# Performance work log

Hardware: AMD Instinct MI355X
Metric: run time of the kernel (lower is better)

Reference implementation:

```python
import jax, jax.numpy as jnp
import numpy as np

B, S = 4, 4096          # batch, tokens (64x64 SAM ViT-H grid)
DIN, DOUT = 1280, 3840  # qkv linear dims
RANK = 16
NUM_SHARED = 1
NUM_ROUTED = 6
TOP_K = 3


def setup_inputs() -> dict:
    key = jax.random.key(0)
    ks = jax.random.split(key, 9)
    s = 0.02
    return {
        "x": jax.random.normal(ks[0], (B, S, DIN), dtype=jnp.float32),
        "base_w": jax.random.normal(ks[1], (DIN, DOUT), dtype=jnp.float32) * s,
        "base_b": jax.random.normal(ks[2], (DOUT,), dtype=jnp.float32) * s,
        "shared_w1": jax.random.normal(ks[3], (NUM_SHARED, DIN, RANK), dtype=jnp.float32) * s,
        "shared_w2": jax.random.normal(ks[4], (NUM_SHARED, RANK, DOUT), dtype=jnp.float32) * s,
        "routed_w1": jax.random.normal(ks[5], (NUM_ROUTED, DIN, RANK), dtype=jnp.float32) * s,
        "routed_w2": jax.random.normal(ks[6], (NUM_ROUTED, RANK, DOUT), dtype=jnp.float32) * s,
        "router_w": jax.random.normal(ks[7], (DIN, NUM_ROUTED), dtype=jnp.float32) * s,
        "router_b": jax.random.normal(ks[8], (NUM_ROUTED,), dtype=jnp.float32) * s,
    }


def reference(x, base_w, base_b, shared_w1, shared_w2, routed_w1, routed_w2, router_w, router_b):
    b, s, din = x.shape
    # base linear runs under torch.no_grad() -> stop_gradient
    base = jax.lax.stop_gradient(jnp.einsum('bsi,io->bso', x, base_w) + base_b)
    # shared low-rank experts, summed over the shared set
    shared = jnp.einsum('bsi,eir,ero->bso', x, shared_w1, shared_w2)
    # router: softmax gates, top-k selection
    gates = jax.nn.softmax(x @ router_w + router_b, axis=-1)      # [B,S,E]
    topk_w, topk_idx = jax.lax.top_k(gates, TOP_K)                # [B,S,K]
    T = b * s
    xf = x.reshape(T, din)
    # combine weights: per-token weight for each expert (top-k indices are
    # distinct, so scatter-add reproduces the per-slot assignment exactly)
    cw = jnp.zeros((T, NUM_ROUTED), dtype=x.dtype).at[
        jnp.arange(T)[:, None], topk_idx.reshape(T, TOP_K)
    ].add(topk_w.reshape(T, TOP_K))                               # [T,E]
    # routed experts: contract rank and expert dims without materializing [T,E,DOUT]
    h = jnp.einsum('ti,eir->ter', xf, routed_w1)                  # [T,E,RANK]
    routed = jnp.einsum('ter,ero,te->to', h, routed_w2, cw).reshape(b, s, DOUT)
    return base + shared + routed
```

## Files before the change

### kernel.cpp

```cpp
#include <hip/hip_runtime.h>
#include <cstdint>
#include <cstddef>

#define DIN 1280
#define DOUT 3840
#define NEXP 6
#define RANK 16
#define TOKENS 16384
#define KPAD 1408
#define NLOW 128

typedef __bf16 bf16x8 __attribute__((ext_vector_type(8)));
typedef float f32x4 __attribute__((ext_vector_type(4)));
typedef unsigned short u16x8 __attribute__((ext_vector_type(8)));

#define SB() __builtin_amdgcn_sched_barrier(0)
#define BAR() __builtin_amdgcn_s_barrier()

__device__ __forceinline__ unsigned short f2bf(float f) {
    unsigned u = __builtin_bit_cast(unsigned, f);
    u += 0x7fff + ((u >> 16) & 1);
    return (unsigned short)(u >> 16);
}

__device__ __forceinline__ void async_load16(void* lds, const void* g) {
    __builtin_amdgcn_global_load_lds(
        (const __attribute__((address_space(1))) unsigned int*)g,
        (__attribute__((address_space(3))) unsigned int*)lds, 16, 0, 0);
}

__global__ void prep_w2t(const float* __restrict__ base_w,
                         const float* __restrict__ shared_w2,
                         const float* __restrict__ routed_w2,
                         unsigned short* __restrict__ WT) {
    __shared__ unsigned short tile[32][33];
    int k0 = blockIdx.x * 32, n0 = blockIdx.y * 32;
    int tx = threadIdx.x, ty = threadIdx.y;
#pragma unroll
    for (int j = 0; j < 4; j++) {
        int k = k0 + ty + j * 8;
        int n = n0 + tx;
        float v;
        if (k < DIN)            v = base_w[(size_t)k * DOUT + n];
        else if (k < DIN + 16)  v = shared_w2[(size_t)(k - DIN) * DOUT + n];
        else if (k < DIN + 112) v = routed_w2[(size_t)(k - DIN - 16) * DOUT + n];
        else                    v = 0.f;
        tile[ty + j * 8][tx] = f2bf(v);
    }
    __syncthreads();
#pragma unroll
    for (int j = 0; j < 4; j++) {
        int n = n0 + ty + j * 8;
        int k = k0 + tx;
        WT[(size_t)n * KPAD + k] = tile[tx][ty + j * 8];
    }
}

__global__ void prep_w1t(const float* __restrict__ shared_w1,
                         const float* __restrict__ routed_w1,
                         unsigned short* __restrict__ W1T) {
    __shared__ unsigned short tile[32][33];
    int k0 = blockIdx.x * 32, n0 = blockIdx.y * 32;
    int tx = threadIdx.x, ty = threadIdx.y;
#pragma unroll
    for (int j = 0; j < 4; j++) {
        int k = k0 + ty + j * 8;
        int n = n0 + tx;
        float v = 0.f;
        if (n < 16) v = shared_w1[k * RANK + n];
        else if (n < 112) {
            int jj = n - 16, e = jj >> 4, r = jj & 15;
            v = routed_w1[(size_t)e * DIN * RANK + k * RANK + r];
        }
        tile[ty + j * 8][tx] = f2bf(v);
    }
    __syncthreads();
#pragma unroll
    for (int j = 0; j < 4; j++) {
        int n = n0 + ty + j * 8;
        int k = k0 + tx;
        W1T[(size_t)n * DIN + k] = tile[tx][ty + j * 8];
    }
}

__global__ __launch_bounds__(256) void router_kernel(
    const float* __restrict__ x,
    const float* __restrict__ router_w,
    const float* __restrict__ router_b,
    unsigned short* __restrict__ A,
    float* __restrict__ cw) {
    int tid = threadIdx.x;
    size_t t0 = (size_t)blockIdx.x * 8;
    const float* xblk = x + t0 * DIN;
    unsigned short* Ablk = A + t0 * KPAD;

    for (int i = tid; i < 8 * (DIN / 8); i += 256) {
        int t = i / (DIN / 8), c = (i - t * (DIN / 8)) * 8;
        const float* xs = xblk + (size_t)t * DIN + c;
        f32x4 v0 = *(const f32x4*)xs;
        f32x4 v1 = *(const f32x4*)(xs + 4);
        u16x8 o;
#pragma unroll
        for (int j = 0; j < 4; j++) { o[j] = f2bf(v0[j]); o[4 + j] = f2bf(v1[j]); }
        *(u16x8*)&Ablk[(size_t)t * KPAD + c] = o;
    }
    if (tid < 128) {
        int t = tid >> 4, c = tid & 15;
        Ablk[t * KPAD + DIN + 112 + c] = 0;
    }

    int tg = tid >> 5, lj = tid & 31;
    const float* xt = xblk + (size_t)tg * DIN;
    float acc[6] = {0.f, 0.f, 0.f, 0.f, 0.f, 0.f};
    for (int k = lj; k < DIN; k += 32) {
        float xv = xt[k];
        const float* wr = router_w + k * NEXP;
#pragma unroll
        for (int e = 0; e < NEXP; e++) acc[e] = fmaf(xv, wr[e], acc[e]);
    }
#pragma unroll
    for (int off = 16; off > 0; off >>= 1)
#pragma unroll
        for (int e = 0; e < NEXP; e++) acc[e] += __shfl_xor(acc[e], off);

    float mx = -1e30f;
#pragma unroll
    for (int e = 0; e < NEXP; e++) { acc[e] += router_b[e]; mx = fmaxf(mx, acc[e]); }
    float g[6]; float s = 0.f;
#pragma unroll
    for (int e = 0; e < NEXP; e++) { g[e] = __expf(acc[e] - mx); s += g[e]; }
    float inv = 1.f / s;
    if (lj < NEXP) {
        float ge = g[lj];
        int cnt = 0;
#pragma unroll
        for (int e = 0; e < NEXP; e++) {
            if (e == lj) continue;
            if (g[e] > ge || (g[e] == ge && e < lj)) cnt++;
        }
        cw[(t0 + tg) * NEXP + lj] = (cnt < 3) ? ge * inv : 0.f;
    }
}

__global__ __launch_bounds__(256) void combine_kernel(
    const float* __restrict__ H, const float* __restrict__ cw,
    unsigned short* __restrict__ A) {
    int i = blockIdx.x * 256 + threadIdx.x;
    int t = i / 112, j = i - t * 112;
    float h = H[(size_t)t * NLOW + j] + H[(size_t)TOKENS * NLOW + (size_t)t * NLOW + j];
    float f = (j < 16) ? 1.0f : cw[t * NEXP + ((j - 16) >> 4)];
    A[(size_t)t * KPAD + DIN + j] = f2bf(f * h);
}

__global__ __launch_bounds__(256, 2) void gemm_small(
    const unsigned short* __restrict__ A,
    const unsigned short* __restrict__ BT,
    float* __restrict__ H) {
    __shared__ unsigned short ldsA[128 * 32];
    __shared__ unsigned short ldsB[128 * 32];
    const int KS = DIN / 2;
    int tid = threadIdx.x;
    int lane = tid & 63, wave = tid >> 6;
    int m0 = blockIdx.y * 128;
    int z = blockIdx.z;
    int wm = (wave >> 1) * 64, wn = (wave & 1) * 64;
    int lr = lane & 15, quad = lane >> 4;

    f32x4 acc[4][4] = {};
    const unsigned short* Abase = A + (size_t)m0 * KPAD + z * KS;
    const unsigned short* Bbase = BT + z * KS;
    float* Cbase = H + (size_t)z * TOKENS * NLOW;

    for (int k0 = 0; k0 < KS; k0 += 32) {
#pragma unroll
        for (int i = 0; i < 2; i++) {
            int c = i * 256 + tid;
            int row = c >> 2;
            int col = (c & 3) << 3;
            async_load16(&ldsA[(i * 256 + wave * 64) * 8],
                         Abase + (size_t)row * KPAD + k0 + col);
            async_load16(&ldsB[(i * 256 + wave * 64) * 8],
                         Bbase + (size_t)row * DIN + k0 + col);
        }
        __syncthreads();
        bf16x8 af[4], bf[4];
#pragma unroll
        for (int mi = 0; mi < 4; mi++)
            af[mi] = *(const bf16x8*)&ldsA[(wm + mi * 16 + lr) * 32 + quad * 8];
#pragma unroll
        for (int ni = 0; ni < 4; ni++)
            bf[ni] = *(const bf16x8*)&ldsB[(wn + ni * 16 + lr) * 32 + quad * 8];
#pragma unroll
        for (int mi = 0; mi < 4; mi++)
#pragma unroll
            for (int ni = 0; ni < 4; ni++)
                acc[mi][ni] = __builtin_amdgcn_mfma_f32_16x16x32_bf16(
                    af[mi], bf[ni], acc[mi][ni], 0, 0, 0);
        __syncthreads();
    }
#pragma unroll
    for (int ni = 0; ni < 4; ni++) {
        int gn = wn + ni * 16 + lr;
#pragma unroll
        for (int mi = 0; mi < 4; mi++) {
            int gm = m0 + wm + mi * 16 + quad * 4;
            f32x4 v = acc[mi][ni];
#pragma unroll
            for (int r = 0; r < 4; r++)
                Cbase[(size_t)(gm + r) * NLOW + gn] = v[r];
        }
    }
}


#define READ_AQ(AQ, MB) do { \
    AQ[0][0] = rdA(a_cur, (MB) + 0, 0); AQ[0][1] = rdA(a_cur, (MB) + 0, 1); \
    AQ[1][0] = rdA(a_cur, (MB) + 1, 0); AQ[1][1] = rdA(a_cur, (MB) + 1, 1); \
} while (0)

#define MFMA_QUAD(AQ, MB) do { \
    _Pragma("unroll") for (int ks_ = 0; ks_ < 2; ks_++) \
    _Pragma("unroll") for (int mq_ = 0; mq_ < 2; mq_++) \
    _Pragma("unroll") for (int ni_ = 0; ni_ < 4; ni_++) \
        acc[(MB) + mq_][ni_] = __builtin_amdgcn_mfma_f32_16x16x32_bf16( \
            AQ[mq_][ks_], bfr[ni_][ks_], acc[(MB) + mq_][ni_], 0, 0, 0); \
} while (0)

__global__ __launch_bounds__(512, 2) void gemm256(
    const unsigned short* __restrict__ A,
    const unsigned short* __restrict__ BT,
    const float* __restrict__ bias,
    float* __restrict__ C) {
    __shared__ unsigned short lA[2][256 * 64];
    __shared__ unsigned short lB[2][256 * 64];

    int tid = threadIdx.x;
    int lane = tid & 63, wave = tid >> 6;
    int bid = blockIdx.x;
    int xcd = bid & 7, lid = bid >> 3;
    int mt = xcd * 8 + (lid & 7);
    int nt = lid >> 3;
    int m0 = mt * 256, n0 = nt * 256;

    int wm = (wave >> 2) * 128, wn = (wave & 3) * 64;
    int lr = lane & 15, quad = lane >> 4;
    int swz = (lr & 7) << 4;

    int sr = lane >> 3;
    int sc = (lane & 7) ^ sr;
    const unsigned short* aSrc = A + (size_t)(m0 + wave * 32 + sr) * KPAD + sc * 8;
    const unsigned short* bSrc = BT + (size_t)(n0 + wave * 32 + sr) * KPAD + sc * 8;

    auto stA4 = [&](unsigned short* dst, int k0) {
#pragma unroll
        for (int i = 0; i < 4; i++)
            async_load16(dst + (size_t)(wave * 32 + i * 8) * 64,
                         aSrc + (size_t)(i * 8) * KPAD + k0);
    };
    auto stB1 = [&](unsigned short* dst, int k0, int i) {
        async_load16(dst + (size_t)(wave * 32 + i * 8) * 64,
                     bSrc + (size_t)(i * 8) * KPAD + k0);
    };
    auto rdA = [&](const unsigned short* base, int mi, int ks) -> bf16x8 {
        int row = wm + mi * 16 + lr;
        int off = row * 128 + (((ks << 6) | (quad << 4)) ^ swz);
        return *(const bf16x8*)((const char*)base + off);
    };
    auto rdB = [&](const unsigned short* base, int ni, int ks) -> bf16x8 {
        int row = wn + ni * 16 + lr;
        int off = row * 128 + (((ks << 6) | (quad << 4)) ^ swz);
        return *(const bf16x8*)((const char*)base + off);
    };

    f32x4 acc[8][4] = {};

    stA4(&lA[0][0], 0);
#pragma unroll
    for (int i = 0; i < 4; i++) stB1(&lB[0][0], 0, i);
#pragma unroll
    for (int i = 0; i < 4; i++) stB1(&lB[1][0], 64, i);
    asm volatile("s_waitcnt vmcnt(4)" ::: "memory");
    SB(); BAR(); SB();

    const int nkt = KPAD / 64;
#pragma unroll 2
    for (int t = 0; t < nkt; ++t) {
        const int ct = t & 1;
        unsigned short* a_cur = &lA[ct][0];
        unsigned short* b_cur = &lB[ct][0];
        unsigned short* a_nxt = &lA[ct ^ 1][0];
        int k0 = t * 64;

        bf16x8 bfr[4][2];
#pragma unroll
        for (int ni = 0; ni < 4; ni++) {
            bfr[ni][0] = rdB(b_cur, ni, 0);
            bfr[ni][1] = rdB(b_cur, ni, 1);
        }
        SB();
        bf16x8 aq0[2][2], aq1[2][2], aq2[2][2], aq3[2][2];
        READ_AQ(aq0, 0);
        READ_AQ(aq1, 2);
        if (t + 1 < nkt) stA4(a_nxt, k0 + 64);

        READ_AQ(aq2, 4);
        __builtin_amdgcn_s_setprio(1); MFMA_QUAD(aq0, 0); __builtin_amdgcn_s_setprio(0);
        asm volatile("s_waitcnt lgkmcnt(8)" ::: "memory");
        SB(); BAR(); SB();

        READ_AQ(aq3, 6);
        if (t + 2 < nkt) { stB1(b_cur, k0 + 128, 0); stB1(b_cur, k0 + 128, 1); }
        __builtin_amdgcn_s_setprio(1); MFMA_QUAD(aq1, 2); __builtin_amdgcn_s_setprio(0);

        if (t + 2 < nkt) { stB1(b_cur, k0 + 128, 2); stB1(b_cur, k0 + 128, 3); }
        __builtin_amdgcn_s_setprio(1); MFMA_QUAD(aq2, 4); __builtin_amdgcn_s_setprio(0);

        __builtin_amdgcn_s_setprio(1); MFMA_QUAD(aq3, 6); __builtin_amdgcn_s_setprio(0);

        if (t + 2 < nkt) asm volatile("s_waitcnt vmcnt(4) lgkmcnt(0)" ::: "memory");
        else             asm volatile("s_waitcnt vmcnt(0) lgkmcnt(0)" ::: "memory");
        SB(); BAR(); SB();
    }

#pragma unroll
    for (int mi = 0; mi < 8; mi++) {
        int gm = m0 + wm + mi * 16 + quad * 4;
#pragma unroll
        for (int ni = 0; ni < 4; ni++) {
            int gn = n0 + wn + ni * 16 + lr;
            float bv = bias[gn];
            f32x4 v = acc[mi][ni];
#pragma unroll
            for (int r = 0; r < 4; r++)
                C[(size_t)(gm + r) * DOUT + gn] = v[r] + bv;
        }
    }
}

extern "C" void kernel_launch(void* const* d_in, const int* in_sizes, int n_in,
                              void* d_out, int out_size, void* d_ws, size_t ws_size,
                              hipStream_t stream) {
    const float* x         = (const float*)d_in[0];
    const float* base_w    = (const float*)d_in[1];
    const float* base_b    = (const float*)d_in[2];
    const float* shared_w1 = (const float*)d_in[3];
    const float* shared_w2 = (const float*)d_in[4];
    const float* routed_w1 = (const float*)d_in[5];
    const float* routed_w2 = (const float*)d_in[6];
    const float* router_w  = (const float*)d_in[7];
    const float* router_b  = (const float*)d_in[8];
    float* out = (float*)d_out;

    char* ws = (char*)d_ws;
    size_t off = 0;
    unsigned short* A     = (unsigned short*)(ws + off); off += (size_t)TOKENS * KPAD * 2;
    unsigned short* WcatT = (unsigned short*)(ws + off); off += (size_t)DOUT * KPAD * 2;
    unsigned short* W1T   = (unsigned short*)(ws + off); off += (size_t)NLOW * DIN * 2;
    float* H              = (float*)(ws + off);          off += (size_t)2 * TOKENS * NLOW * 4;
    float* cw             = (float*)(ws + off);          off += (size_t)TOKENS * NEXP * 4;

    prep_w2t<<<dim3(KPAD / 32, DOUT / 32), dim3(32, 8), 0, stream>>>(
        base_w, shared_w2, routed_w2, WcatT);
    prep_w1t<<<dim3(DIN / 32, NLOW / 32), dim3(32, 8), 0, stream>>>(
        shared_w1, routed_w1, W1T);
    router_kernel<<<TOKENS / 8, 256, 0, stream>>>(x, router_w, router_b, A, cw);
    gemm_small<<<dim3(1, TOKENS / 128, 2), 256, 0, stream>>>(A, W1T, H);
    combine_kernel<<<(TOKENS * 112) / 256, 256, 0, stream>>>(H, cw, A);
    gemm256<<<(TOKENS / 256) * (DOUT / 256), 512, 0, stream>>>(A, WcatT, base_b, out);
}
```

Before: 284.9 us.

## Load GEMM B fragments directly to registers and fuse router bf16 conversion with logits

The main GEMM no longer stages the B (weight) tile through LDS. Each wave loads its B fragments straight from global memory into registers, double-buffered one k-tile ahead. This halves LDS use and drops the hand-tuned waitcnt/sched_barrier pipeline for plain __syncthreads. The cost is redundant global loads of B across the two M-waves and loss of the fine-grained MFMA/load interleaving. The router kernel now reads each token's x once, producing both the bf16 copy and the router dot products in one pass instead of two.

```diff
diff --git a/kernel.cpp b/kernel.cpp
--- a/kernel.cpp
+++ b/kernel.cpp
@@ -13,9 +13,6 @@
 typedef __bf16 bf16x8 __attribute__((ext_vector_type(8)));
 typedef float f32x4 __attribute__((ext_vector_type(4)));
 typedef unsigned short u16x8 __attribute__((ext_vector_type(8)));
-
-#define SB() __builtin_amdgcn_sched_barrier(0)
-#define BAR() __builtin_amdgcn_s_barrier()
 
 __device__ __forceinline__ unsigned short f2bf(float f) {
     unsigned u = __builtin_bit_cast(unsigned, f);
@@ -91,33 +88,34 @@
     float* __restrict__ cw) {
     int tid = threadIdx.x;
     size_t t0 = (size_t)blockIdx.x * 8;
-    const float* xblk = x + t0 * DIN;
-    unsigned short* Ablk = A + t0 * KPAD;
-
-    for (int i = tid; i < 8 * (DIN / 8); i += 256) {
-        int t = i / (DIN / 8), c = (i - t * (DIN / 8)) * 8;
-        const float* xs = xblk + (size_t)t * DIN + c;
-        f32x4 v0 = *(const f32x4*)xs;
-        f32x4 v1 = *(const f32x4*)(xs + 4);
+    int tg = tid >> 5, lj = tid & 31;
+    const float* xt = x + (t0 + tg) * DIN;
+    unsigned short* At = A + (t0 + tg) * KPAD;
+
+    float acc[6] = {0.f, 0.f, 0.f, 0.f, 0.f, 0.f};
+#pragma unroll
+    for (int cc = 0; cc < 5; cc++) {
+        int c = (lj + cc * 32) * 8;
+        f32x4 v0 = *(const f32x4*)(xt + c);
+        f32x4 v1 = *(const f32x4*)(xt + c + 4);
         u16x8 o;
 #pragma unroll
         for (int j = 0; j < 4; j++) { o[j] = f2bf(v0[j]); o[4 + j] = f2bf(v1[j]); }
-        *(u16x8*)&Ablk[(size_t)t * KPAD + c] = o;
+        *(u16x8*)&At[c] = o;
+        const float* rw = router_w + (size_t)c * NEXP;
+#pragma unroll
+        for (int j = 0; j < 8; j++) {
+            float xv = (j < 4) ? v0[j] : v1[j - 4];
+#pragma unroll
+            for (int e = 0; e < NEXP; e++)
+                acc[e] = fmaf(xv, rw[j * NEXP + e], acc[e]);
+        }
     }
     if (tid < 128) {
-        int t = tid >> 4, c = tid & 15;
-        Ablk[t * KPAD + DIN + 112 + c] = 0;
-    }
-
-    int tg = tid >> 5, lj = tid & 31;
-    const float* xt = xblk + (size_t)tg * DIN;
-    float acc[6] = {0.f, 0.f, 0.f, 0.f, 0.f, 0.f};
-    for (int k = lj; k < DIN; k += 32) {
-        float xv = xt[k];
-        const float* wr = router_w + k * NEXP;
-#pragma unroll
-        for (int e = 0; e < NEXP; e++) acc[e] = fmaf(xv, wr[e], acc[e]);
-    }
+        int t = tid >> 4, cz = tid & 15;
+        A[(t0 + t) * KPAD + DIN + 112 + cz] = 0;
+    }
+
 #pragma unroll
     for (int off = 16; off > 0; off >>= 1)
 #pragma unroll
@@ -213,17 +211,29 @@
 }
 
 
-#define READ_AQ(AQ, MB) do { \
-    AQ[0][0] = rdA(a_cur, (MB) + 0, 0); AQ[0][1] = rdA(a_cur, (MB) + 0, 1); \
-    AQ[1][0] = rdA(a_cur, (MB) + 1, 0); AQ[1][1] = rdA(a_cur, (MB) + 1, 1); \
-} while (0)
-
-#define MFMA_QUAD(AQ, MB) do { \
-    _Pragma("unroll") for (int ks_ = 0; ks_ < 2; ks_++) \
-    _Pragma("unroll") for (int mq_ = 0; mq_ < 2; mq_++) \
-    _Pragma("unroll") for (int ni_ = 0; ni_ < 4; ni_++) \
-        acc[(MB) + mq_][ni_] = __builtin_amdgcn_mfma_f32_16x16x32_bf16( \
-            AQ[mq_][ks_], bfr[ni_][ks_], acc[(MB) + mq_][ni_], 0, 0, 0); \
+#define NKT 22
+
+#define GTILE(CUR, BRC, BRN) do { \
+    const int t_ = 2 * tt + (CUR); \
+    if (t_ + 1 < NKT) { stA(&lA[(CUR) ^ 1][0], (t_ + 1) * 64); ldB(BRN, t_ + 1); } \
+    const unsigned short* a_cur = &lA[CUR][0]; \
+    _Pragma("unroll") \
+    for (int q = 0; q < 4; q++) { \
+        bf16x8 a00 = rdA(a_cur, q * 2 + 0, 0), a01 = rdA(a_cur, q * 2 + 0, 1); \
+        bf16x8 a10 = rdA(a_cur, q * 2 + 1, 0), a11 = rdA(a_cur, q * 2 + 1, 1); \
+        _Pragma("unroll") \
+        for (int ni = 0; ni < 4; ni++) { \
+            acc[q * 2 + 0][ni] = __builtin_amdgcn_mfma_f32_16x16x32_bf16( \
+                a00, BRC[ni * 2 + 0], acc[q * 2 + 0][ni], 0, 0, 0); \
+            acc[q * 2 + 0][ni] = __builtin_amdgcn_mfma_f32_16x16x32_bf16( \
+                a01, BRC[ni * 2 + 1], acc[q * 2 + 0][ni], 0, 0, 0); \
+            acc[q * 2 + 1][ni] = __builtin_amdgcn_mfma_f32_16x16x32_bf16( \
+                a10, BRC[ni * 2 + 0], acc[q * 2 + 1][ni], 0, 0, 0); \
+            acc[q * 2 + 1][ni] = __builtin_amdgcn_mfma_f32_16x16x32_bf16( \
+                a11, BRC[ni * 2 + 1], acc[q * 2 + 1][ni], 0, 0, 0); \
+        } \
+    } \
+    __syncthreads(); \
 } while (0)
 
 __global__ __launch_bounds__(512, 2) void gemm256(
@@ -232,7 +242,6 @@
     const float* __restrict__ bias,
     float* __restrict__ C) {
     __shared__ unsigned short lA[2][256 * 64];
-    __shared__ unsigned short lB[2][256 * 64];
 
     int tid = threadIdx.x;
     int lane = tid & 63, wave = tid >> 6;
@@ -249,77 +258,38 @@
     int sr = lane >> 3;
     int sc = (lane & 7) ^ sr;
     const unsigned short* aSrc = A + (size_t)(m0 + wave * 32 + sr) * KPAD + sc * 8;
-    const unsigned short* bSrc = BT + (size_t)(n0 + wave * 32 + sr) * KPAD + sc * 8;
-
-    auto stA4 = [&](unsigned short* dst, int k0) {
+    const unsigned short* bPtr = BT + (size_t)(n0 + wn + lr) * KPAD + quad * 8;
+
+    auto stA = [&](unsigned short* dst, int k0) {
 #pragma unroll
         for (int i = 0; i < 4; i++)
             async_load16(dst + (size_t)(wave * 32 + i * 8) * 64,
                          aSrc + (size_t)(i * 8) * KPAD + k0);
-    };
-    auto stB1 = [&](unsigned short* dst, int k0, int i) {
-        async_load16(dst + (size_t)(wave * 32 + i * 8) * 64,
-                     bSrc + (size_t)(i * 8) * KPAD + k0);
     };
     auto rdA = [&](const unsigned short* base, int mi, int ks) -> bf16x8 {
         int row = wm + mi * 16 + lr;
         int off = row * 128 + (((ks << 6) | (quad << 4)) ^ swz);
         return *(const bf16x8*)((const char*)base + off);
     };
-    auto rdB = [&](const unsigned short* base, int ni, int ks) -> bf16x8 {
-        int row = wn + ni * 16 + lr;
-        int off = row * 128 + (((ks << 6) | (quad << 4)) ^ swz);
-        return *(const bf16x8*)((const char*)base + off);
+    auto ldB = [&](bf16x8* dst, int t) {
+#pragma unroll
+        for (int ni = 0; ni < 4; ni++)
+#pragma unroll
+            for (int ks = 0; ks < 2; ks++)
+                dst[ni * 2 + ks] = *(const bf16x8*)(
+                    bPtr + (size_t)(ni * 16) * KPAD + t * 64 + ks * 32);
     };
 
     f32x4 acc[8][4] = {};
-
-    stA4(&lA[0][0], 0);
-#pragma unroll
-    for (int i = 0; i < 4; i++) stB1(&lB[0][0], 0, i);
-#pragma unroll
-    for (int i = 0; i < 4; i++) stB1(&lB[1][0], 64, i);
-    asm volatile("s_waitcnt vmcnt(4)" ::: "memory");
-    SB(); BAR(); SB();
-
-    const int nkt = KPAD / 64;
-#pragma unroll 2
-    for (int t = 0; t < nkt; ++t) {
-        const int ct = t & 1;
-        unsigned short* a_cur = &lA[ct][0];
-        unsigned short* b_cur = &lB[ct][0];
-        unsigned short* a_nxt = &lA[ct ^ 1][0];
-        int k0 = t * 64;
-
-        bf16x8 bfr[4][2];
-#pragma unroll
-        for (int ni = 0; ni < 4; ni++) {
-            bfr[ni][0] = rdB(b_cur, ni, 0);
-            bfr[ni][1] = rdB(b_cur, ni, 1);
-        }
-        SB();
-        bf16x8 aq0[2][2], aq1[2][2], aq2[2][2], aq3[2][2];
-        READ_AQ(aq0, 0);
-        READ_AQ(aq1, 2);
-        if (t + 1 < nkt) stA4(a_nxt, k0 + 64);
-
-        READ_AQ(aq2, 4);
-        __builtin_amdgcn_s_setprio(1); MFMA_QUAD(aq0, 0); __builtin_amdgcn_s_setprio(0);
-        asm volatile("s_waitcnt lgkmcnt(8)" ::: "memory");
-        SB(); BAR(); SB();
-
-        READ_AQ(aq3, 6);
-        if (t + 2 < nkt) { stB1(b_cur, k0 + 128, 0); stB1(b_cur, k0 + 128, 1); }
-        __builtin_amdgcn_s_setprio(1); MFMA_QUAD(aq1, 2); __builtin_amdgcn_s_setprio(0);
-
-        if (t + 2 < nkt) { stB1(b_cur, k0 + 128, 2); stB1(b_cur, k0 + 128, 3); }
-        __builtin_amdgcn_s_setprio(1); MFMA_QUAD(aq2, 4); __builtin_amdgcn_s_setprio(0);
-
-        __builtin_amdgcn_s_setprio(1); MFMA_QUAD(aq3, 6); __builtin_amdgcn_s_setprio(0);
-
-        if (t + 2 < nkt) asm volatile("s_waitcnt vmcnt(4) lgkmcnt(0)" ::: "memory");
-        else             asm volatile("s_waitcnt vmcnt(0) lgkmcnt(0)" ::: "memory");
-        SB(); BAR(); SB();
+    bf16x8 br0[8], br1[8];
+
+    stA(&lA[0][0], 0);
+    ldB(br0, 0);
+    __syncthreads();
+
+    for (int tt = 0; tt < NKT / 2; ++tt) {
+        GTILE(0, br0, br1);
+        GTILE(1, br1, br0);
     }
 
 #pragma unroll
@@ -366,5 +336,6 @@
     router_kernel<<<TOKENS / 8, 256, 0, stream>>>(x, router_w, router_b, A, cw);
     gemm_small<<<dim3(1, TOKENS / 128, 2), 256, 0, stream>>>(A, W1T, H);
     combine_kernel<<<(TOKENS * 112) / 256, 256, 0, stream>>>(H, cw, A);
-    gemm256<<<(TOKENS / 256) * (DOUT / 256), 512, 0, stream>>>(A, WcatT, base_b, out);
-}
+    gemm256<<<(TOKENS / 256) * (DOUT / 256), 512, 0, stream>>>(
+        A, WcatT, base_b, out);
+}
```

Measured after the change: 363.6 us. 27.7% more time.
